# Performance work log

Hardware: AMD Instinct MI355X
Metric: run time of the kernel (lower is better)

Reference implementation:

```python
import jax, jax.numpy as jnp
import numpy as np

D_MODEL = 1024
NUM_HEADS = 16
HEAD_DIM = D_MODEL // NUM_HEADS


def setup_inputs() -> dict:
    key = jax.random.key(0)
    ks = jax.random.split(key, 7)
    B, S = 2, 2048
    scale = 1.0 / np.sqrt(D_MODEL)
    inp = {
        "input": jax.random.normal(ks[0], (B, S, D_MODEL), dtype=jnp.float32),
        "W_q": jax.random.normal(ks[1], (D_MODEL, D_MODEL), dtype=jnp.float32) * scale,
        "b_q": jax.random.normal(ks[2], (D_MODEL,), dtype=jnp.float32) * 0.01,
        "W_k": jax.random.normal(ks[3], (D_MODEL, D_MODEL), dtype=jnp.float32) * scale,
        "b_k": jax.random.normal(ks[4], (D_MODEL,), dtype=jnp.float32) * 0.01,
        "W_v": jax.random.normal(ks[5], (D_MODEL, D_MODEL), dtype=jnp.float32) * scale,
        "b_v": jax.random.normal(ks[6], (D_MODEL,), dtype=jnp.float32) * 0.01,
    }
    return inp


def reference(input, W_q, b_q, W_k, b_k, W_v, b_v):
    B, S, _ = input.shape
    # QKV projections (torch nn.Linear: x @ W^T + b); split heads -> [B,H,S,Dh]
    def proj(W, b):
        y = jnp.einsum('bsd,ed->bse', input, W) + b
        return y.reshape(B, S, NUM_HEADS, HEAD_DIM).transpose(0, 2, 1, 3)

    Q = proj(W_q, b_q)
    K = proj(W_k, b_k)
    V = proj(W_v, b_v)

    scores = jnp.einsum('bhqd,bhkd->bhqk', Q, K) / jnp.sqrt(
        jnp.asarray(HEAD_DIM, dtype=input.dtype))
    attention_weights = jax.nn.softmax(scores, axis=-1)  # [B,H,S,S]
    out = jnp.einsum('bhqk,bhkd->bhqd', attention_weights, V)
    out = out.transpose(0, 2, 1, 3).reshape(B, S, D_MODEL)
    return out, attention_weights
```

## Files before the change

kernel.cpp:

```cpp
#include <hip/hip_runtime.h>
#include <stdint.h>

#define S_LEN   2048
#define D_MODEL 1024
#define N_HEADS 16
#define HEAD_D  64
#define BATCH   2
#define M_TOT   (BATCH * S_LEN)

typedef __attribute__((ext_vector_type(8))) short s8v;
typedef __attribute__((ext_vector_type(4))) float f4v;
typedef __attribute__((ext_vector_type(4))) unsigned short u4v;

__device__ __forceinline__ float bf2f(unsigned short u) {
    union { unsigned int i; float f; } c; c.i = ((unsigned int)u) << 16; return c.f;
}
__device__ __forceinline__ unsigned short f2bf(float f) {
    union { float f; unsigned int i; } c; c.f = f;
    unsigned int u = c.i + 0x7FFFu + ((c.i >> 16) & 1u);
    return (unsigned short)(u >> 16);
}
__device__ __forceinline__ unsigned int pk2bf(float lo, float hi) {
    return (unsigned int)f2bf(lo) | ((unsigned int)f2bf(hi) << 16);
}
__device__ __forceinline__ float hw_exp2(float x) { return __builtin_amdgcn_exp2f(x); }

#define GLD16(gp, lp) __builtin_amdgcn_global_load_lds(                      \
    (const __attribute__((address_space(1))) void*)(const void*)(gp),        \
    (__attribute__((address_space(3))) void*)(void*)(lp), 16, 0, 0)

#define BAR_LGKM() asm volatile("s_waitcnt lgkmcnt(0)\n\ts_barrier" ::: "memory")

#define EXP_SCALE 0.1803368801111204f

__global__ __launch_bounds__(256) void cvt_bf16(const float* __restrict__ src,
                                                unsigned short* __restrict__ dst, int n) {
    int i = (blockIdx.x * 256 + threadIdx.x) * 4;
    int stride = gridDim.x * 1024;
    for (; i < n; i += stride) {
        float4 v = *(const float4*)(src + i);
        u4v o;
        o[0] = f2bf(v.x); o[1] = f2bf(v.y); o[2] = f2bf(v.z); o[3] = f2bf(v.w);
        *(u4v*)(dst + i) = o;
    }
}

__global__ __launch_bounds__(256) void qkv_gemm(
    const unsigned short* __restrict__ X,
    const unsigned short* __restrict__ Wq, const unsigned short* __restrict__ Wk,
    const unsigned short* __restrict__ Wv,
    const float* __restrict__ bq, const float* __restrict__ bk, const float* __restrict__ bv,
    unsigned short* __restrict__ q_ws, unsigned short* __restrict__ k_ws,
    unsigned short* __restrict__ vt_ws) {
    __shared__ unsigned short sA[128 * 32];
    __shared__ unsigned short sB[128 * 32];

    const int z = blockIdx.z;
    const unsigned short* Wm = (z == 0) ? Wq : ((z == 1) ? Wk : Wv);
    const float* bm = (z == 0) ? bq : ((z == 1) ? bk : bv);
    const int m0 = blockIdx.x * 128, n0 = blockIdx.y * 128;
    const int t = threadIdx.x;
    const int lane = t & 63, w = t >> 6;
    const int fr = lane & 15, g = lane >> 4;
    const int wr = w >> 1, wc = w & 1;

    f4v acc[4][4];
#pragma unroll
    for (int i = 0; i < 4; ++i)
#pragma unroll
        for (int j = 0; j < 4; ++j) acc[i][j] = (f4v){0.f, 0.f, 0.f, 0.f};

    const int rowL = t >> 2;
    const int colL = (t & 3) * 8;
    const unsigned short* gA = X + (size_t)(m0 + rowL) * D_MODEL + colL;
    const unsigned short* gB = Wm + (size_t)(n0 + rowL) * D_MODEL + colL;

    for (int kb = 0; kb < 32; ++kb) {
        const int k0 = kb * 32;
        GLD16(gA + k0,                 sA + w * 512);
        GLD16(gA + 64 * D_MODEL + k0,  sA + 2048 + w * 512);
        GLD16(gB + k0,                 sB + w * 512);
        GLD16(gB + 64 * D_MODEL + k0,  sB + 2048 + w * 512);
        __syncthreads();

        s8v af[4], bfv[4];
#pragma unroll
        for (int i = 0; i < 4; ++i)
            af[i] = *(const s8v*)(sA + (wr * 64 + i * 16 + fr) * 32 + g * 8);
#pragma unroll
        for (int j = 0; j < 4; ++j)
            bfv[j] = *(const s8v*)(sB + (wc * 64 + j * 16 + fr) * 32 + g * 8);
#pragma unroll
        for (int i = 0; i < 4; ++i)
#pragma unroll
            for (int j = 0; j < 4; ++j)
                acc[i][j] = __builtin_amdgcn_mfma_f32_16x16x32_bf16(af[i], bfv[j], acc[i][j], 0, 0, 0);
        __syncthreads();
    }

    const int e_base = n0 + wc * 64;
    const int m_base = m0 + wr * 64;
    if (z < 2) {
        unsigned short* dst = (z == 0) ? q_ws : k_ws;
#pragma unroll
        for (int i = 0; i < 4; ++i) {
#pragma unroll
            for (int j = 0; j < 4; ++j) {
                const int e = e_base + j * 16 + fr;
                const int h = e >> 6, dh = e & 63;
                const float bias = bm[e];
                const int mr = m_base + i * 16 + g * 4;
                const int b_ = mr >> 11, srow = mr & 2047;
                const size_t base = (((size_t)(b_ * N_HEADS + h) * S_LEN + srow) << 6) + dh;
#pragma unroll
                for (int r = 0; r < 4; ++r)
                    dst[base + ((size_t)r << 6)] = f2bf(acc[i][j][r] + bias);
            }
        }
    } else {
#pragma unroll
        for (int i = 0; i < 4; ++i) {
#pragma unroll
            for (int j = 0; j < 4; ++j) {
                const int e = e_base + j * 16 + fr;
                const int h = e >> 6, dh = e & 63;
                const float bias = bm[e];
                const int mr = m_base + i * 16 + g * 4;
                const int b_ = mr >> 11, srow = mr & 2047;
                u4v pk;
#pragma unroll
                for (int r = 0; r < 4; ++r) pk[r] = f2bf(acc[i][j][r] + bias);
                *(u4v*)(vt_ws + ((size_t)(b_ * N_HEADS + h) * HEAD_D + dh) * S_LEN + srow) = pk;
            }
        }
    }
}

__global__ __launch_bounds__(256, 2) void attn_fused8(
    const unsigned short* __restrict__ q_ws, const unsigned short* __restrict__ k_ws,
    const unsigned short* __restrict__ vt_ws,
    float* __restrict__ out, float* __restrict__ wts) {
    __shared__ __align__(16) char SM[81920];

    const int t = threadIdx.x, lane = t & 63, w = t >> 6;
    const int fr = lane & 15, g = lane >> 4;
    const int blk = blockIdx.x;
    const int bh = (blk & 7) * 4 + (blk >> 7);
    const int tp = (blk >> 3) & 15;
    const int q0 = tp * 128 + w * 16;
    const int q1 = q0 + 64;

    const unsigned short* Kp = k_ws + (size_t)bh * S_LEN * HEAD_D;
    const unsigned short* Vt = vt_ws + (size_t)bh * HEAD_D * S_LEN;
    const unsigned short* Qp0 = q_ws + ((size_t)bh * S_LEN + q0) * HEAD_D;
    const unsigned short* Qp1 = q_ws + ((size_t)bh * S_LEN + q1) * HEAD_D;

    const s8v qa00 = *(const s8v*)(Qp0 + fr * HEAD_D + g * 8);
    const s8v qa01 = *(const s8v*)(Qp0 + fr * HEAD_D + 32 + g * 8);
    const s8v qa10 = *(const s8v*)(Qp1 + fr * HEAD_D + g * 8);
    const s8v qa11 = *(const s8v*)(Qp1 + fr * HEAD_D + 32 + g * 8);

    auto stageK128 = [&](int c, char* dst) {
#pragma unroll
        for (int j = 0; j < 4; ++j) {
            const int d = t * 16 + j * 4096;
            const int row = d >> 7, cb = (d >> 4) & 7;
            GLD16(Kp + (size_t)(c * 128 + row) * HEAD_D + ((cb ^ (row & 7)) << 3),
                  dst + w * 1024 + j * 4096);
        }
    };
    auto stageV128 = [&](int c, char* dst) {
#pragma unroll
        for (int j = 0; j < 4; ++j) {
            const int d = t * 16 + j * 4096;
            const int row = d >> 8, cb = (d >> 4) & 15;
            GLD16(Vt + (size_t)row * S_LEN + c * 128 + ((cb ^ (row & 15)) << 3),
                  dst + w * 1024 + j * 4096);
        }
    };
    auto qk16 = [&](const char* kb, int st, const s8v& a0, const s8v& a1) -> f4v {
        const int row = st * 16 + fr, m = row & 7;
        const s8v ka0 = *(const s8v*)(kb + row * 128 + ((g ^ m) << 4));
        const s8v ka1 = *(const s8v*)(kb + row * 128 + (((4 + g) ^ m) << 4));
        f4v s = (f4v){0.f, 0.f, 0.f, 0.f};
        s = __builtin_amdgcn_mfma_f32_16x16x32_bf16(ka0, a0, s, 0, 0, 0);
        s = __builtin_amdgcn_mfma_f32_16x16x32_bf16(ka1, a1, s, 0, 0, 0);
        return s;
    };

    char* PL = SM + 65536 + w * 4096;
    const int b_ = bh >> 4, h = bh & 15;
    const int r0 = lane >> 4, cc = lane & 15;

    auto passB_iter = [&](const char* kb, const char* vl, float inv,
                          const s8v& a0, const s8v& a1, float* wbase, int c,
                          f4v* acc, float* rs_other, const s8v* o0, const s8v* o1) {
#pragma unroll
        for (int st = 0; st < 8; ++st) {
            const f4v s = qk16(kb, st, a0, a1);
            f4v p;
#pragma unroll
            for (int r = 0; r < 4; ++r) p[r] = hw_exp2(s[r] * EXP_SCALE) * inv;
            const int bix = st * 2 + (g >> 1);
            const int wa = fr * 256 + (((bix ^ fr) << 4) | ((g & 1) * 8));
            *(unsigned int*)(PL + wa)     = pk2bf(p[0], p[1]);
            *(unsigned int*)(PL + wa + 4) = pk2bf(p[2], p[3]);
        }
#pragma unroll
        for (int i = 0; i < 4; ++i) {
            const int row = i * 4 + r0;
#pragma unroll
            for (int grp = 0; grp < 2; ++grp) {
                const int bir = grp * 8 + (cc >> 1);
                const u4v pw = *(const u4v*)(PL + row * 256 +
                                             (((bir ^ row) << 4) | ((cc & 1) * 8)));
                f4v o;
#pragma unroll
                for (int e = 0; e < 4; ++e) o[e] = bf2f(pw[e]);
                __builtin_nontemporal_store(o,
                    (f4v*)(wbase + (size_t)row * S_LEN + c * 128 + grp * 64 + cc * 4));
            }
        }
        if (rs_other) {
            float acc_rs = 0.f;
#pragma unroll
            for (int st = 0; st < 8; ++st) {
                const f4v s = qk16(kb, st, *o0, *o1);
#pragma unroll
                for (int r = 0; r < 4; ++r) acc_rs += hw_exp2(s[r] * EXP_SCALE);
            }
            *rs_other += acc_rs;
        }
#pragma unroll
        for (int ks = 0; ks < 4; ++ks) {
            const s8v pa = *(const s8v*)(PL + fr * 256 + (((ks * 4 + g) ^ fr) << 4));
#pragma unroll
            for (int tt = 0; tt < 4; ++tt) {
                const int vrow = tt * 16 + fr;
                const s8v vv = *(const s8v*)(vl + vrow * 256 +
                                             (((ks * 4 + g) ^ (vrow & 15)) << 4));
                acc[tt] = __builtin_amdgcn_mfma_f32_16x16x32_bf16(pa, vv, acc[tt], 0, 0, 0);
            }
        }
    };

    float rsum0 = 0.f;
    stageK128(0, SM);
    for (int c = 0; c < 16; ++c) {
        const int cur = c & 1;
        if (c < 15) stageK128(c + 1, SM + (cur ^ 1) * 16384);
        if (c < 15) asm volatile("s_waitcnt vmcnt(4)" ::: "memory");
        else        asm volatile("s_waitcnt vmcnt(0)" ::: "memory");
        asm volatile("s_barrier" ::: "memory");
        const char* kb = SM + cur * 16384;
#pragma unroll
        for (int st = 0; st < 8; ++st) {
            const f4v s = qk16(kb, st, qa00, qa01);
#pragma unroll
            for (int r = 0; r < 4; ++r) rsum0 += hw_exp2(s[r] * EXP_SCALE);
        }
        BAR_LGKM();
    }
    rsum0 += __shfl_xor(rsum0, 16);
    rsum0 += __shfl_xor(rsum0, 32);
    const float inv0 = 1.f / rsum0;

    f4v acc[4];
#pragma unroll
    for (int i = 0; i < 4; ++i) acc[i] = (f4v){0.f, 0.f, 0.f, 0.f};
    float rsum1 = 0.f;
    float* wbase0 = wts + ((size_t)bh * S_LEN + q0) * S_LEN;

    stageK128(0, SM); stageV128(0, SM + 32768);
    for (int c = 0; c < 16; ++c) {
        const int cur = c & 1;
        if (c < 15) { stageK128(c + 1, SM + (cur ^ 1) * 16384);
                      stageV128(c + 1, SM + 32768 + (cur ^ 1) * 16384); }
        if (c == 0)      asm volatile("s_waitcnt vmcnt(8)" ::: "memory");
        else if (c < 15) asm volatile("s_waitcnt vmcnt(16)" ::: "memory");
        else             asm volatile("s_waitcnt vmcnt(8)" ::: "memory");
        asm volatile("s_barrier" ::: "memory");
        passB_iter(SM + cur * 16384, SM + 32768 + cur * 16384, inv0,
                   qa00, qa01, wbase0, c, acc, &rsum1, &qa10, &qa11);
        BAR_LGKM();
    }
    rsum1 += __shfl_xor(rsum1, 16);
    rsum1 += __shfl_xor(rsum1, 32);
    const float inv1 = 1.f / rsum1;

#pragma unroll
    for (int tt = 0; tt < 4; ++tt)
#pragma unroll
        for (int r = 0; r < 4; ++r)
            __builtin_nontemporal_store(acc[tt][r],
                &out[((size_t)b_ * S_LEN + q0 + g * 4 + r) * D_MODEL +
                     h * HEAD_D + tt * 16 + fr]);

#pragma unroll
    for (int i = 0; i < 4; ++i) acc[i] = (f4v){0.f, 0.f, 0.f, 0.f};
    float* wbase1 = wts + ((size_t)bh * S_LEN + q1) * S_LEN;

    stageK128(0, SM); stageV128(0, SM + 32768);
    for (int c = 0; c < 16; ++c) {
        const int cur = c & 1;
        if (c < 15) { stageK128(c + 1, SM + (cur ^ 1) * 16384);
                      stageV128(c + 1, SM + 32768 + (cur ^ 1) * 16384); }
        if (c == 0)      asm volatile("s_waitcnt vmcnt(8)" ::: "memory");
        else if (c < 15) asm volatile("s_waitcnt vmcnt(16)" ::: "memory");
        else             asm volatile("s_waitcnt vmcnt(8)" ::: "memory");
        asm volatile("s_barrier" ::: "memory");
        passB_iter(SM + cur * 16384, SM + 32768 + cur * 16384, inv1,
                   qa10, qa11, wbase1, c, acc, nullptr, nullptr, nullptr);
        BAR_LGKM();
    }

#pragma unroll
    for (int tt = 0; tt < 4; ++tt)
#pragma unroll
        for (int r = 0; r < 4; ++r)
            __builtin_nontemporal_store(acc[tt][r],
                &out[((size_t)b_ * S_LEN + q1 + g * 4 + r) * D_MODEL +
                     h * HEAD_D + tt * 16 + fr]);
}

extern "C" void kernel_launch(void* const* d_in, const int* in_sizes, int n_in,
                              void* d_out, int out_size, void* d_ws, size_t ws_size,
                              hipStream_t stream) {
    const float* x  = (const float*)d_in[0];
    const float* Wq = (const float*)d_in[1];
    const float* bq = (const float*)d_in[2];
    const float* Wk = (const float*)d_in[3];
    const float* bk = (const float*)d_in[4];
    const float* Wv = (const float*)d_in[5];
    const float* bv = (const float*)d_in[6];

    float* out = (float*)d_out;
    float* wts = out + (size_t)BATCH * S_LEN * D_MODEL;

    unsigned short* xb    = (unsigned short*)d_ws;
    unsigned short* wqb   = xb  + (size_t)M_TOT * D_MODEL;
    unsigned short* wkb   = wqb + (size_t)D_MODEL * D_MODEL;
    unsigned short* wvb   = wkb + (size_t)D_MODEL * D_MODEL;
    unsigned short* q_ws  = wvb + (size_t)D_MODEL * D_MODEL;
    unsigned short* k_ws  = q_ws + (size_t)M_TOT * D_MODEL;
    unsigned short* vt_ws = k_ws + (size_t)M_TOT * D_MODEL;

    cvt_bf16<<<1024, 256, 0, stream>>>(x,  xb,  M_TOT * D_MODEL);
    cvt_bf16<<<256,  256, 0, stream>>>(Wq, wqb, D_MODEL * D_MODEL);
    cvt_bf16<<<256,  256, 0, stream>>>(Wk, wkb, D_MODEL * D_MODEL);
    cvt_bf16<<<256,  256, 0, stream>>>(Wv, wvb, D_MODEL * D_MODEL);

    qkv_gemm<<<dim3(32, 8, 3), 256, 0, stream>>>(xb, wqb, wkb, wvb, bq, bk, bv,
                                                 q_ws, k_ws, vt_ws);

    attn_fused8<<<512, 256, 0, stream>>>(q_ws, k_ws, vt_ws, out, wts);
}
```

Before: 185.6 us.

## Compute both query row-sum passes together and share K/V tiles across both query blocks

The row-sum pass now computes softmax denominators for both 16-row query groups per warp in a single sweep over K, using 256-row K tiles. The output pass then loads each K/V tile once and processes both query groups against it, replacing two separate passes over K and V. This removes one full stream of K/V loads from global memory and the QK recompute that was previously interleaved. In exchange the kernel holds two accumulator sets in registers, which raises register pressure under the two-blocks-per-CU launch bound. The vmcnt wait thresholds were also raised to match the larger number of loads in flight.

```diff
diff --git a/kernel.cpp b/kernel.cpp
--- a/kernel.cpp
+++ b/kernel.cpp
@@ -136,7 +136,7 @@
     }
 }
 
-__global__ __launch_bounds__(256, 2) void attn_fused8(
+__global__ __launch_bounds__(256, 2) void attn_fused9(
     const unsigned short* __restrict__ q_ws, const unsigned short* __restrict__ k_ws,
     const unsigned short* __restrict__ vt_ws,
     float* __restrict__ out, float* __restrict__ wts) {
@@ -166,6 +166,15 @@
             const int d = t * 16 + j * 4096;
             const int row = d >> 7, cb = (d >> 4) & 7;
             GLD16(Kp + (size_t)(c * 128 + row) * HEAD_D + ((cb ^ (row & 7)) << 3),
+                  dst + w * 1024 + j * 4096);
+        }
+    };
+    auto stageK256 = [&](int c, char* dst) {
+#pragma unroll
+        for (int j = 0; j < 8; ++j) {
+            const int d = t * 16 + j * 4096;
+            const int row = d >> 7, cb = (d >> 4) & 7;
+            GLD16(Kp + (size_t)(c * 256 + row) * HEAD_D + ((cb ^ (row & 7)) << 3),
                   dst + w * 1024 + j * 4096);
         }
     };
@@ -192,9 +201,8 @@
     const int b_ = bh >> 4, h = bh & 15;
     const int r0 = lane >> 4, cc = lane & 15;
 
-    auto passB_iter = [&](const char* kb, const char* vl, float inv,
-                          const s8v& a0, const s8v& a1, float* wbase, int c,
-                          f4v* acc, float* rs_other, const s8v* o0, const s8v* o1) {
+    auto do_tile = [&](const char* kb, const char* vl, float inv,
+                       const s8v& a0, const s8v& a1, float* wbase, int c, f4v* acc) {
 #pragma unroll
         for (int st = 0; st < 8; ++st) {
             const f4v s = qk16(kb, st, a0, a1);
@@ -220,16 +228,6 @@
                 __builtin_nontemporal_store(o,
                     (f4v*)(wbase + (size_t)row * S_LEN + c * 128 + grp * 64 + cc * 4));
             }
-        }
-        if (rs_other) {
-            float acc_rs = 0.f;
-#pragma unroll
-            for (int st = 0; st < 8; ++st) {
-                const f4v s = qk16(kb, st, *o0, *o1);
-#pragma unroll
-                for (int r = 0; r < 4; ++r) acc_rs += hw_exp2(s[r] * EXP_SCALE);
-            }
-            *rs_other += acc_rs;
         }
 #pragma unroll
         for (int ks = 0; ks < 4; ++ks) {
@@ -244,32 +242,44 @@
         }
     };
 
-    float rsum0 = 0.f;
-    stageK128(0, SM);
-    for (int c = 0; c < 16; ++c) {
+    float rsum0 = 0.f, rsum1 = 0.f;
+    stageK256(0, SM);
+    for (int c = 0; c < 8; ++c) {
         const int cur = c & 1;
-        if (c < 15) stageK128(c + 1, SM + (cur ^ 1) * 16384);
-        if (c < 15) asm volatile("s_waitcnt vmcnt(4)" ::: "memory");
-        else        asm volatile("s_waitcnt vmcnt(0)" ::: "memory");
+        if (c < 7) stageK256(c + 1, SM + (cur ^ 1) * 32768);
+        if (c < 7) asm volatile("s_waitcnt vmcnt(8)" ::: "memory");
+        else       asm volatile("s_waitcnt vmcnt(0)" ::: "memory");
         asm volatile("s_barrier" ::: "memory");
-        const char* kb = SM + cur * 16384;
-#pragma unroll
-        for (int st = 0; st < 8; ++st) {
+        const char* kb = SM + cur * 32768;
+#pragma unroll
+        for (int st = 0; st < 16; ++st) {
             const f4v s = qk16(kb, st, qa00, qa01);
 #pragma unroll
             for (int r = 0; r < 4; ++r) rsum0 += hw_exp2(s[r] * EXP_SCALE);
+        }
+#pragma unroll
+        for (int st = 0; st < 16; ++st) {
+            const f4v s = qk16(kb, st, qa10, qa11);
+#pragma unroll
+            for (int r = 0; r < 4; ++r) rsum1 += hw_exp2(s[r] * EXP_SCALE);
         }
         BAR_LGKM();
     }
     rsum0 += __shfl_xor(rsum0, 16);
     rsum0 += __shfl_xor(rsum0, 32);
+    rsum1 += __shfl_xor(rsum1, 16);
+    rsum1 += __shfl_xor(rsum1, 32);
     const float inv0 = 1.f / rsum0;
-
-    f4v acc[4];
-#pragma unroll
-    for (int i = 0; i < 4; ++i) acc[i] = (f4v){0.f, 0.f, 0.f, 0.f};
-    float rsum1 = 0.f;
+    const float inv1 = 1.f / rsum1;
+
+    f4v acc0[4], acc1[4];
+#pragma unroll
+    for (int i = 0; i < 4; ++i) {
+        acc0[i] = (f4v){0.f, 0.f, 0.f, 0.f};
+        acc1[i] = (f4v){0.f, 0.f, 0.f, 0.f};
+    }
     float* wbase0 = wts + ((size_t)bh * S_LEN + q0) * S_LEN;
+    float* wbase1 = wts + ((size_t)bh * S_LEN + q1) * S_LEN;
 
     stageK128(0, SM); stageV128(0, SM + 32768);
     for (int c = 0; c < 16; ++c) {
@@ -277,50 +287,27 @@
         if (c < 15) { stageK128(c + 1, SM + (cur ^ 1) * 16384);
                       stageV128(c + 1, SM + 32768 + (cur ^ 1) * 16384); }
         if (c == 0)      asm volatile("s_waitcnt vmcnt(8)" ::: "memory");
-        else if (c < 15) asm volatile("s_waitcnt vmcnt(16)" ::: "memory");
-        else             asm volatile("s_waitcnt vmcnt(8)" ::: "memory");
+        else if (c < 15) asm volatile("s_waitcnt vmcnt(24)" ::: "memory");
+        else             asm volatile("s_waitcnt vmcnt(16)" ::: "memory");
         asm volatile("s_barrier" ::: "memory");
-        passB_iter(SM + cur * 16384, SM + 32768 + cur * 16384, inv0,
-                   qa00, qa01, wbase0, c, acc, &rsum1, &qa10, &qa11);
+        const char* kb = SM + cur * 16384;
+        const char* vl = SM + 32768 + cur * 16384;
+        do_tile(kb, vl, inv0, qa00, qa01, wbase0, c, acc0);
+        do_tile(kb, vl, inv1, qa10, qa11, wbase1, c, acc1);
         BAR_LGKM();
     }
-    rsum1 += __shfl_xor(rsum1, 16);
-    rsum1 += __shfl_xor(rsum1, 32);
-    const float inv1 = 1.f / rsum1;
 
 #pragma unroll
     for (int tt = 0; tt < 4; ++tt)
 #pragma unroll
-        for (int r = 0; r < 4; ++r)
-            __builtin_nontemporal_store(acc[tt][r],
+        for (int r = 0; r < 4; ++r) {
+            __builtin_nontemporal_store(acc0[tt][r],
                 &out[((size_t)b_ * S_LEN + q0 + g * 4 + r) * D_MODEL +
                      h * HEAD_D + tt * 16 + fr]);
-
-#pragma unroll
-    for (int i = 0; i < 4; ++i) acc[i] = (f4v){0.f, 0.f, 0.f, 0.f};
-    float* wbase1 = wts + ((size_t)bh * S_LEN + q1) * S_LEN;
-
-    stageK128(0, SM); stageV128(0, SM + 32768);
-    for (int c = 0; c < 16; ++c) {
-        const int cur = c & 1;
-        if (c < 15) { stageK128(c + 1, SM + (cur ^ 1) * 16384);
-                      stageV128(c + 1, SM + 32768 + (cur ^ 1) * 16384); }
-        if (c == 0)      asm volatile("s_waitcnt vmcnt(8)" ::: "memory");
-        else if (c < 15) asm volatile("s_waitcnt vmcnt(16)" ::: "memory");
-        else             asm volatile("s_waitcnt vmcnt(8)" ::: "memory");
-        asm volatile("s_barrier" ::: "memory");
-        passB_iter(SM + cur * 16384, SM + 32768 + cur * 16384, inv1,
-                   qa10, qa11, wbase1, c, acc, nullptr, nullptr, nullptr);
-        BAR_LGKM();
-    }
-
-#pragma unroll
-    for (int tt = 0; tt < 4; ++tt)
-#pragma unroll
-        for (int r = 0; r < 4; ++r)
-            __builtin_nontemporal_store(acc[tt][r],
+            __builtin_nontemporal_store(acc1[tt][r],
                 &out[((size_t)b_ * S_LEN + q1 + g * 4 + r) * D_MODEL +
                      h * HEAD_D + tt * 16 + fr]);
+        }
 }
 
 extern "C" void kernel_launch(void* const* d_in, const int* in_sizes, int n_in,
@@ -353,5 +340,5 @@
     qkv_gemm<<<dim3(32, 8, 3), 256, 0, stream>>>(xb, wqb, wkb, wvb, bq, bk, bv,
                                                  q_ws, k_ws, vt_ws);
 
-    attn_fused8<<<512, 256, 0, stream>>>(q_ws, k_ws, vt_ws, out, wts);
-}
+    attn_fused9<<<512, 256, 0, stream>>>(q_ws, k_ws, vt_ws, out, wts);
+}
```

Result: slower. 196.5 us (+5.9%).
